# Kernel optimization log

Measured on AMD Instinct MI355X. Metric: run time of the kernel, lower is better.

## Reference

```python
import jax, jax.numpy as jnp
import numpy as np

VOCAB = 50000
EMBED = 256
LABELS = 2
DEPTH = 10          # complete binary tree: 2**DEPTH leaves
B = 256             # batch of trees
L = 2 ** DEPTH      # leaves per tree


def setup_inputs() -> dict:
    key = jax.random.key(0)
    ks = jax.random.split(key, 7)
    token_ids = jax.random.randint(ks[0], (B, L), 0, VOCAB)
    labels = jax.random.randint(ks[1], (B,), 0, LABELS)
    emb = jax.random.normal(ks[2], (VOCAB, EMBED), dtype=jnp.float32)
    W_w = jax.random.normal(ks[3], (EMBED, 2 * EMBED), dtype=jnp.float32) * (1.0 / np.sqrt(2 * EMBED))
    W_b = jax.random.normal(ks[4], (EMBED,), dtype=jnp.float32) * 0.01
    P_w = jax.random.normal(ks[5], (LABELS, EMBED), dtype=jnp.float32) * (1.0 / np.sqrt(EMBED))
    P_b = jax.random.normal(ks[6], (LABELS,), dtype=jnp.float32) * 0.01
    return {"token_ids": token_ids, "labels": labels, "emb": emb,
            "W_w": W_w, "W_b": W_b, "P_w": P_w, "P_b": P_b}


def reference(token_ids, labels, emb, W_w, W_b, P_w, P_b):
    # Leaves: relu(embedding(token))  -> [B, L, E]
    x = jax.nn.relu(emb[token_ids])
    # Level-by-level combine: currentNode = relu(W @ cat(left, right) + b)
    # Leaf order is left-to-right, so adjacent pairs (2k, 2k+1) are siblings;
    # reshape concatenates (left, right) along features, matching torch.cat((l, r), 1).
    while x.shape[1] > 1:
        bsz, n, e = x.shape
        lr = x.reshape(bsz, n // 2, 2 * e)                       # [B, n/2, 2E]
        x = jax.nn.relu(jnp.einsum('bnf,ef->bne', lr, W_w) + W_b)
    root = x[:, 0]                                               # [B, E]
    logits = root @ P_w.T + P_b                                  # [B, label_size]
    prediction = jnp.argmax(logits, axis=1)
    logp = jax.nn.log_softmax(logits, axis=-1)
    loss = -jnp.take_along_axis(logp, labels[:, None], axis=1)[:, 0]  # per-tree CE
    return prediction, loss
```

## Files before the change

kernel.cpp:

```cpp
#include <hip/hip_runtime.h>
#include <hip/hip_bf16.h>
#include <math.h>

#define EMBED   256
#define KDIM    512
#define BATCH   256
#define BM      128
#define VOCAB   50000

typedef float  f32x4   __attribute__((ext_vector_type(4)));
typedef __bf16 bf16x8  __attribute__((ext_vector_type(8)));
typedef unsigned short ushort8 __attribute__((ext_vector_type(8)));

__device__ __forceinline__ unsigned short f2h(float f) {
    unsigned int u = __float_as_uint(f);
    u += 0x7FFFu + ((u >> 16) & 1u);
    return (unsigned short)(u >> 16);
}
__device__ __forceinline__ float h2f(unsigned short h) {
    return __uint_as_float(((unsigned int)h) << 16);
}
__device__ __forceinline__ void gload16(const void* g, void* l) {
    __builtin_amdgcn_global_load_lds(
        (const __attribute__((address_space(1))) unsigned int*)g,
        (__attribute__((address_space(3))) unsigned int*)l, 16, 0, 0);
}

#define MFMA16(a,b,c) __builtin_amdgcn_mfma_f32_16x16x32_bf16((a),(b),(c),0,0,0)

__global__ __launch_bounds__(256) void prep_all(const float* __restrict__ emb,
                                                unsigned short* __restrict__ Eh,
                                                unsigned short* __restrict__ El,
                                                const float* __restrict__ W,
                                                unsigned short* __restrict__ Wh,
                                                unsigned short* __restrict__ Wl,
                                                int wprep)
{
    const int bid = blockIdx.x;
    if (bid < 6250) {
        const size_t base = ((size_t)bid * 256 + threadIdx.x) * 8;
        float v[8];
        *(float4*)&v[0] = *(const float4*)&emb[base];
        *(float4*)&v[4] = *(const float4*)&emb[base + 4];
        ushort8 hs, ls;
        #pragma unroll
        for (int i = 0; i < 8; ++i) {
            const float f = fmaxf(v[i], 0.f);
            const unsigned short h = f2h(f);
            hs[i] = h;
            ls[i] = f2h(f - h2f(h));
        }
        *(ushort8*)&Eh[base] = hs;
        *(ushort8*)&El[base] = ls;
    } else if (wprep) {
        const int i = (bid - 6250) * 256 + threadIdx.x;
        const float w = W[i];
        const unsigned short h = f2h(w);
        Wh[i] = h;
        Wl[i] = f2h(w - h2f(h));
    }
}

template<int LV1, int WPREP>
__global__ __launch_bounds__(512) void gemm_tree(
    const unsigned short* __restrict__ Xh, const unsigned short* __restrict__ Xl,
    const unsigned short* __restrict__ Wh, const unsigned short* __restrict__ Wl,
    const float*  __restrict__ Wf,
    const float*  __restrict__ bias,
    unsigned short* __restrict__ Yh, unsigned short* __restrict__ Yl,
    const int* __restrict__ tok,
    const unsigned short* __restrict__ Eh, const unsigned short* __restrict__ El)
{
    __shared__ __align__(16) unsigned short AhL[4096], AlL[4096];
    __shared__ __align__(16) unsigned short BhL[8192], BlL[8192];

    const int tid = threadIdx.x;
    const int wid = tid >> 6;
    const int l   = tid & 63;
    const int q   = l >> 4;
    const int rr  = l & 15;
    const int m0  = blockIdx.x * BM;

    const int waveM = wid >> 2;
    const int waveN = wid & 3;

    int tk0 = 0, tk1 = 0;
    if constexpr (LV1) {
        const int r = m0 + wid * 16 + rr;
        tk0 = tok[2 * r];
        tk1 = tok[2 * r + 1];
    }

    f32x4 acc[4][4] = {};

    for (int t = 0; t < 16; ++t) {
        const int k0   = t << 5;
        const int joff = k0 >> 8;
        const int c    = (k0 & 255) + q * 8;

        if constexpr (LV1) {
            const size_t off = (size_t)(joff ? tk1 : tk0) * EMBED + c;
            gload16(Eh + off, &AhL[wid * 512]);
            gload16(El + off, &AlL[wid * 512]);
        } else {
            const size_t off = (size_t)(2 * (m0 + wid * 16 + rr) + joff) * EMBED + c;
            gload16(Xh + off, &AhL[wid * 512]);
            gload16(Xl + off, &AlL[wid * 512]);
        }
        #pragma unroll
        for (int g = 0; g < 2; ++g) {
            const int s = wid + g * 8;
            if constexpr (WPREP) {
                const size_t off = (size_t)(s * 16 + rr) * KDIM + k0 + q * 8;
                gload16(Wh + off, &BhL[s * 512]);
                gload16(Wl + off, &BlL[s * 512]);
            } else {
                const float* ws = Wf + (size_t)(s * 16 + rr) * KDIM + k0 + q * 8;
                float v[8];
                *(float4*)&v[0] = *(const float4*)ws;
                *(float4*)&v[4] = *(const float4*)(ws + 4);
                ushort8 hs, ls;
                #pragma unroll
                for (int i = 0; i < 8; ++i) {
                    const unsigned short h = f2h(v[i]);
                    hs[i] = h;
                    ls[i] = f2h(v[i] - h2f(h));
                }
                *(ushort8*)&BhL[s * 512 + l * 8] = hs;
                *(ushort8*)&BlL[s * 512 + l * 8] = ls;
            }
        }

        __syncthreads();

        bf16x8 ah[4], al[4], bh[4], bl[4];
        #pragma unroll
        for (int mi = 0; mi < 4; ++mi) {
            ah[mi] = *(const bf16x8*)&AhL[(waveM * 4 + mi) * 512 + l * 8];
            al[mi] = *(const bf16x8*)&AlL[(waveM * 4 + mi) * 512 + l * 8];
        }
        #pragma unroll
        for (int ni = 0; ni < 4; ++ni) {
            bh[ni] = *(const bf16x8*)&BhL[(waveN * 4 + ni) * 512 + l * 8];
            bl[ni] = *(const bf16x8*)&BlL[(waveN * 4 + ni) * 512 + l * 8];
        }
        #pragma unroll
        for (int mi = 0; mi < 4; ++mi)
            #pragma unroll
            for (int ni = 0; ni < 4; ++ni)
                acc[mi][ni] = MFMA16(ah[mi], bh[ni], acc[mi][ni]);
        #pragma unroll
        for (int mi = 0; mi < 4; ++mi)
            #pragma unroll
            for (int ni = 0; ni < 4; ++ni)
                acc[mi][ni] = MFMA16(al[mi], bh[ni], acc[mi][ni]);
        #pragma unroll
        for (int mi = 0; mi < 4; ++mi)
            #pragma unroll
            for (int ni = 0; ni < 4; ++ni)
                acc[mi][ni] = MFMA16(ah[mi], bl[ni], acc[mi][ni]);

        __syncthreads();
    }

    #pragma unroll
    for (int ni = 0; ni < 4; ++ni) {
        const int col = waveN * 64 + ni * 16 + rr;
        const float bv = bias[col];
        #pragma unroll
        for (int mi = 0; mi < 4; ++mi) {
            const int row0 = m0 + waveM * 64 + mi * 16 + q * 4;
            #pragma unroll
            for (int jj = 0; jj < 4; ++jj) {
                const float y = fmaxf(acc[mi][ni][jj] + bv, 0.f);
                const unsigned short h = f2h(y);
                Yh[(size_t)(row0 + jj) * EMBED + col] = h;
                Yl[(size_t)(row0 + jj) * EMBED + col] = f2h(y - h2f(h));
            }
        }
    }
}

template<int WPREP>
__global__ __launch_bounds__(256) void tail3(
    const unsigned short* __restrict__ A2h, const unsigned short* __restrict__ A2l,
    unsigned short* __restrict__ S3h, unsigned short* __restrict__ S3l,
    const unsigned short* __restrict__ Wh, const unsigned short* __restrict__ Wl,
    const float* __restrict__ Wf, const float* __restrict__ bias,
    const float* __restrict__ Pw, const float* __restrict__ Pb,
    const int* __restrict__ labels, float* __restrict__ out)
{
    __shared__ __align__(16) unsigned short BhT[2][8192], BlT[2][8192];
    __shared__ __align__(16) unsigned short Asth[2][4096], Astl[2][4096];
    __shared__ __align__(16) unsigned short X0h[8192], X0l[8192];
    __shared__ __align__(16) unsigned short X1h[4096], X1l[4096];

    const int tid = threadIdx.x;
    const int w   = tid >> 6;
    const int l   = tid & 63;
    const int q   = l >> 4;
    const int rr  = l & 15;
    const int b   = blockIdx.x;

    unsigned short* L4h = S3h + (size_t)32768 * 256;
    unsigned short* L4l = S3l + (size_t)32768 * 256;

    auto stageB = [&](int buf, int k0) {
        if constexpr (WPREP) {
            #pragma unroll
            for (int j = 0; j < 8; ++j) {
                const int sb = w * 8 + j;
                const int s  = sb & 15;
                const size_t off = (size_t)(s * 16 + rr) * KDIM + k0 + q * 8;
                if (sb < 16) gload16(Wh + off, &BhT[buf][s * 512]);
                else         gload16(Wl + off, &BlT[buf][s * 512]);
            }
        } else {
            #pragma unroll
            for (int j = 0; j < 4; ++j) {
                const int u = w * 4 + j;
                const float* ws = Wf + (size_t)(u * 16 + rr) * KDIM + k0 + q * 8;
                float v[8];
                *(float4*)&v[0] = *(const float4*)ws;
                *(float4*)&v[4] = *(const float4*)(ws + 4);
                ushort8 hs, ls;
                #pragma unroll
                for (int i = 0; i < 8; ++i) {
                    const unsigned short h = f2h(v[i]);
                    hs[i] = h;
                    ls[i] = f2h(v[i] - h2f(h));
                }
                *(ushort8*)&BhT[buf][u * 512 + l * 8] = hs;
                *(ushort8*)&BlT[buf][u * 512 + l * 8] = ls;
            }
        }
    };

    float bv[4];
    #pragma unroll
    for (int ni = 0; ni < 4; ++ni) bv[ni] = bias[w * 64 + ni * 16 + rr];

    int g = 0;

    auto stageA3 = [&](int buf, int t) {
        const int k0 = t * 32, joff = k0 >> 8, c = (k0 & 255) + q * 8;
        #pragma unroll
        for (int j = 0; j < 4; ++j) {
            const int u = w * 4 + j, s = u & 7;
            const size_t off = (size_t)(256 * b + 2 * (s * 16 + rr) + joff) * EMBED + c;
            if (u < 8) gload16(A2h + off, &Asth[buf][s * 512]);
            else       gload16(A2l + off, &Astl[buf][s * 512]);
        }
    };
    stageB(0, 0);
    stageA3(0, 0);
    __syncthreads();
    {
        f32x4 acc[8][4] = {};
        for (int t = 0; t < 16; ++t, ++g) {
            const int cur = g & 1;
            if (g < 127) stageB(cur ^ 1, ((t + 1) & 15) * 32);
            if (t < 15)  stageA3((t + 1) & 1, t + 1);
            bf16x8 bh4[4], bl4[4];
            #pragma unroll
            for (int ni = 0; ni < 4; ++ni) {
                bh4[ni] = *(const bf16x8*)&BhT[cur][(w * 4 + ni) * 512 + l * 8];
                bl4[ni] = *(const bf16x8*)&BlT[cur][(w * 4 + ni) * 512 + l * 8];
            }
            #pragma unroll
            for (int mi = 0; mi < 8; ++mi) {
                const bf16x8 a_h = *(const bf16x8*)&Asth[t & 1][mi * 512 + l * 8];
                const bf16x8 a_l = *(const bf16x8*)&Astl[t & 1][mi * 512 + l * 8];
                #pragma unroll
                for (int ni = 0; ni < 4; ++ni) acc[mi][ni] = MFMA16(a_h, bh4[ni], acc[mi][ni]);
                #pragma unroll
                for (int ni = 0; ni < 4; ++ni) acc[mi][ni] = MFMA16(a_l, bh4[ni], acc[mi][ni]);
                #pragma unroll
                for (int ni = 0; ni < 4; ++ni) acc[mi][ni] = MFMA16(a_h, bl4[ni], acc[mi][ni]);
            }
            __syncthreads();
        }
        #pragma unroll
        for (int ni = 0; ni < 4; ++ni) {
            const int col = w * 64 + ni * 16 + rr;
            #pragma unroll
            for (int mi = 0; mi < 8; ++mi)
                #pragma unroll
                for (int jj = 0; jj < 4; ++jj) {
                    const int row = mi * 16 + q * 4 + jj;
                    const float y = fmaxf(acc[mi][ni][jj] + bv[ni], 0.f);
                    const unsigned short h = f2h(y);
                    S3h[(size_t)(128 * b + row) * EMBED + col] = h;
                    S3l[(size_t)(128 * b + row) * EMBED + col] = f2h(y - h2f(h));
                }
        }
    }
    __syncthreads();

    auto stageA4 = [&](int buf, int t) {
        const int k0 = t * 32, joff = k0 >> 8, c = (k0 & 255) + q * 8;
        #pragma unroll
        for (int j = 0; j < 2; ++j) {
            const int u = w * 2 + j, s = u & 3;
            const size_t off = (size_t)(128 * b + 2 * (s * 16 + rr) + joff) * EMBED + c;
            if (u < 4) gload16(S3h + off, &Asth[buf][s * 512]);
            else       gload16(S3l + off, &Astl[buf][s * 512]);
        }
    };
    stageA4(0, 0);
    {
        f32x4 acc[4][4] = {};
        for (int t = 0; t < 16; ++t, ++g) {
            const int cur = g & 1;
            if (g < 127) stageB(cur ^ 1, ((t + 1) & 15) * 32);
            if (t < 15)  stageA4((t + 1) & 1, t + 1);
            bf16x8 bh4[4], bl4[4];
            #pragma unroll
            for (int ni = 0; ni < 4; ++ni) {
                bh4[ni] = *(const bf16x8*)&BhT[cur][(w * 4 + ni) * 512 + l * 8];
                bl4[ni] = *(const bf16x8*)&BlT[cur][(w * 4 + ni) * 512 + l * 8];
            }
            #pragma unroll
            for (int mi = 0; mi < 4; ++mi) {
                const bf16x8 a_h = *(const bf16x8*)&Asth[t & 1][mi * 512 + l * 8];
                const bf16x8 a_l = *(const bf16x8*)&Astl[t & 1][mi * 512 + l * 8];
                #pragma unroll
                for (int ni = 0; ni < 4; ++ni) acc[mi][ni] = MFMA16(a_h, bh4[ni], acc[mi][ni]);
                #pragma unroll
                for (int ni = 0; ni < 4; ++ni) acc[mi][ni] = MFMA16(a_l, bh4[ni], acc[mi][ni]);
                #pragma unroll
                for (int ni = 0; ni < 4; ++ni) acc[mi][ni] = MFMA16(a_h, bl4[ni], acc[mi][ni]);
            }
            __syncthreads();
        }
        #pragma unroll
        for (int ni = 0; ni < 4; ++ni) {
            const int col = w * 64 + ni * 16 + rr;
            #pragma unroll
            for (int mi = 0; mi < 4; ++mi)
                #pragma unroll
                for (int jj = 0; jj < 4; ++jj) {
                    const int row = mi * 16 + q * 4 + jj;
                    const float y = fmaxf(acc[mi][ni][jj] + bv[ni], 0.f);
                    const unsigned short h = f2h(y);
                    L4h[(size_t)(64 * b + row) * EMBED + col] = h;
                    L4l[(size_t)(64 * b + row) * EMBED + col] = f2h(y - h2f(h));
                }
        }
    }
    __syncthreads();

    auto stageA5 = [&](int buf, int t) {
        const int k0 = t * 32, joff = k0 >> 8, c = (k0 & 255) + q * 8;
        const int u = w, s = u & 1;
        const size_t off = (size_t)(64 * b + 2 * (s * 16 + rr) + joff) * EMBED + c;
        if (u < 2) gload16(L4h + off, &Asth[buf][s * 512]);
        else       gload16(L4l + off, &Astl[buf][s * 512]);
    };
    stageA5(0, 0);
    {
        f32x4 acc[2][4] = {};
        for (int t = 0; t < 16; ++t, ++g) {
            const int cur = g & 1;
            if (g < 127) stageB(cur ^ 1, ((t + 1) & 15) * 32);
            if (t < 15)  stageA5((t + 1) & 1, t + 1);
            bf16x8 bh4[4], bl4[4];
            #pragma unroll
            for (int ni = 0; ni < 4; ++ni) {
                bh4[ni] = *(const bf16x8*)&BhT[cur][(w * 4 + ni) * 512 + l * 8];
                bl4[ni] = *(const bf16x8*)&BlT[cur][(w * 4 + ni) * 512 + l * 8];
            }
            #pragma unroll
            for (int mi = 0; mi < 2; ++mi) {
                const bf16x8 a_h = *(const bf16x8*)&Asth[t & 1][mi * 512 + l * 8];
                const bf16x8 a_l = *(const bf16x8*)&Astl[t & 1][mi * 512 + l * 8];
                #pragma unroll
                for (int ni = 0; ni < 4; ++ni) acc[mi][ni] = MFMA16(a_h, bh4[ni], acc[mi][ni]);
                #pragma unroll
                for (int ni = 0; ni < 4; ++ni) acc[mi][ni] = MFMA16(a_l, bh4[ni], acc[mi][ni]);
                #pragma unroll
                for (int ni = 0; ni < 4; ++ni) acc[mi][ni] = MFMA16(a_h, bl4[ni], acc[mi][ni]);
            }
            __syncthreads();
        }
        #pragma unroll
        for (int ni = 0; ni < 4; ++ni) {
            const int col = w * 64 + ni * 16 + rr;
            #pragma unroll
            for (int mi = 0; mi < 2; ++mi)
                #pragma unroll
                for (int jj = 0; jj < 4; ++jj) {
                    const int row = mi * 16 + q * 4 + jj;
                    const float y = fmaxf(acc[mi][ni][jj] + bv[ni], 0.f);
                    const unsigned short h = f2h(y);
                    const int idx = (row * 256 + col) ^ ((row & 7) << 3);
                    X0h[idx] = h;
                    X0l[idx] = f2h(y - h2f(h));
                }
        }
    }
    __syncthreads();

    for (int s = 1; s < 6; ++s) {
        unsigned short* srch = (s & 1) ? X0h : X1h;
        unsigned short* srcl = (s & 1) ? X0l : X1l;
        unsigned short* dsth = (s & 1) ? X1h : X0h;
        unsigned short* dstl = (s & 1) ? X1l : X0l;
        const int Mout = 32 >> s;

        f32x4 acc[4] = {};
        for (int t = 0; t < 16; ++t, ++g) {
            const int cur = g & 1;
            if (g < 127) stageB(cur ^ 1, ((t + 1) & 15) * 32);

            const int k0   = t * 32;
            const int joff = k0 >> 8;
            const int c    = (k0 & 255) + q * 8;
            const int row  = 2 * rr + joff;
            const int idx  = (row * 256 + c) ^ ((row & 7) << 3);
            const bf16x8 a_h = *(const bf16x8*)&srch[idx];
            const bf16x8 a_l = *(const bf16x8*)&srcl[idx];

            bf16x8 bh4[4], bl4[4];
            #pragma unroll
            for (int ni = 0; ni < 4; ++ni) {
                bh4[ni] = *(const bf16x8*)&BhT[cur][(w * 4 + ni) * 512 + l * 8];
                bl4[ni] = *(const bf16x8*)&BlT[cur][(w * 4 + ni) * 512 + l * 8];
            }
            #pragma unroll
            for (int ni = 0; ni < 4; ++ni) acc[ni] = MFMA16(a_h, bh4[ni], acc[ni]);
            #pragma unroll
            for (int ni = 0; ni < 4; ++ni) acc[ni] = MFMA16(a_l, bh4[ni], acc[ni]);
            #pragma unroll
            for (int ni = 0; ni < 4; ++ni) acc[ni] = MFMA16(a_h, bl4[ni], acc[ni]);

            __syncthreads();
        }

        #pragma unroll
        for (int ni = 0; ni < 4; ++ni) {
            const int col = w * 64 + ni * 16 + rr;
            #pragma unroll
            for (int jj = 0; jj < 4; ++jj) {
                const int row = q * 4 + jj;
                if (row < Mout) {
                    const float y = fmaxf(acc[ni][jj] + bv[ni], 0.f);
                    const unsigned short h = f2h(y);
                    const int idx = (row * 256 + col) ^ ((row & 7) << 3);
                    dsth[idx] = h;
                    dstl[idx] = f2h(y - h2f(h));
                }
            }
        }
        __syncthreads();
    }

    if (w == 0) {
        float s0 = 0.f, s1 = 0.f;
        #pragma unroll
        for (int i = 0; i < 4; ++i) {
            const int col = l + i * 64;
            const float x = h2f(X1h[col]) + h2f(X1l[col]);
            s0 = fmaf(x, Pw[col], s0);
            s1 = fmaf(x, Pw[EMBED + col], s1);
        }
        #pragma unroll
        for (int off = 32; off > 0; off >>= 1) {
            s0 += __shfl_down(s0, off);
            s1 += __shfl_down(s1, off);
        }
        if (l == 0) {
            const float l0 = s0 + Pb[0];
            const float l1 = s1 + Pb[1];
            const int pred = (l1 > l0) ? 1 : 0;
            const float m  = fmaxf(l0, l1);
            const float lse = m + logf(expf(l0 - m) + expf(l1 - m));
            const int lab = labels[b];
            out[b]         = (float)pred;
            out[BATCH + b] = lse - (lab ? l1 : l0);
        }
    }
}

extern "C" void kernel_launch(void* const* d_in, const int* in_sizes, int n_in,
                              void* d_out, int out_size, void* d_ws, size_t ws_size,
                              hipStream_t stream)
{
    const int*   token_ids = (const int*)d_in[0];
    const int*   labels    = (const int*)d_in[1];
    const float* emb       = (const float*)d_in[2];
    const float* W_w       = (const float*)d_in[3];
    const float* W_b       = (const float*)d_in[4];
    const float* P_w       = (const float*)d_in[5];
    const float* P_b       = (const float*)d_in[6];
    float*       out       = (float*)d_out;

    unsigned short* Ah_buf = (unsigned short*)d_ws;
    unsigned short* Al_buf = Ah_buf + (size_t)131072 * 256;
    unsigned short* Bh_buf = Al_buf + (size_t)131072 * 256;
    unsigned short* Bl_buf = Bh_buf + (size_t)65536 * 256;
    unsigned short* Wh     = Bl_buf + (size_t)65536 * 256;
    unsigned short* Wl     = Wh + 131072;
    unsigned short* Eh     = Bh_buf;
    unsigned short* El     = Bl_buf;

    const size_t need_wprep = ((size_t)131072 * 256 * 2 + (size_t)65536 * 256 * 2 + 2 * 131072) * 2;
    const bool wprep = ws_size >= need_wprep;

    prep_all<<<6762, 256, 0, stream>>>(emb, Eh, El, W_w, Wh, Wl, wprep ? 1 : 0);

    if (wprep) {
        gemm_tree<1,1><<<1024, 512, 0, stream>>>(nullptr, nullptr, Wh, Wl, W_w, W_b, Ah_buf, Al_buf, token_ids, Eh, El);
        gemm_tree<0,1><<< 512, 512, 0, stream>>>(Ah_buf, Al_buf, Wh, Wl, W_w, W_b, Bh_buf, Bl_buf, nullptr, nullptr, nullptr);
        tail3<1><<<BATCH, 256, 0, stream>>>(Bh_buf, Bl_buf, Ah_buf, Al_buf, Wh, Wl, W_w, W_b, P_w, P_b, labels, out);
    } else {
        gemm_tree<1,0><<<1024, 512, 0, stream>>>(nullptr, nullptr, Wh, Wl, W_w, W_b, Ah_buf, Al_buf, token_ids, Eh, El);
        gemm_tree<0,0><<< 512, 512, 0, stream>>>(Ah_buf, Al_buf, Wh, Wl, W_w, W_b, Bh_buf, Bl_buf, nullptr, nullptr, nullptr);
        tail3<0><<<BATCH, 256, 0, stream>>>(Bh_buf, Bl_buf, Ah_buf, Al_buf, Wh, Wl, W_w, W_b, P_w, P_b, labels, out);
    }
}
```

Baseline: 409.6 us.

## Widen tail kernel to 8 waves and load operands directly into registers

The per-tree tail kernel now launches 512 threads (8 waves) instead of 256 and splits each level's GEMM across a 2x4 wave grid in M and N. The LDS double-buffered staging of weights and activations is removed, and each wave now reads W and A fragments straight from global memory into registers, which also drops the per-step __syncthreads. The aim is more parallelism per tree and less barrier overhead. In exchange, every wave re-reads the weights from global or cache with no LDS reuse, and the small tree levels split the N dimension across all 8 waves.

```diff
diff --git a/kernel.cpp b/kernel.cpp
--- a/kernel.cpp
+++ b/kernel.cpp
@@ -182,7 +182,7 @@
 }
 
 template<int WPREP>
-__global__ __launch_bounds__(256) void tail3(
+__global__ __launch_bounds__(512) void tail3(
     const unsigned short* __restrict__ A2h, const unsigned short* __restrict__ A2l,
     unsigned short* __restrict__ S3h, unsigned short* __restrict__ S3l,
     const unsigned short* __restrict__ Wh, const unsigned short* __restrict__ Wl,
@@ -190,8 +190,6 @@
     const float* __restrict__ Pw, const float* __restrict__ Pb,
     const int* __restrict__ labels, float* __restrict__ out)
 {
-    __shared__ __align__(16) unsigned short BhT[2][8192], BlT[2][8192];
-    __shared__ __align__(16) unsigned short Asth[2][4096], Astl[2][4096];
     __shared__ __align__(16) unsigned short X0h[8192], X0l[8192];
     __shared__ __align__(16) unsigned short X1h[4096], X1l[4096];
 
@@ -205,21 +203,18 @@
     unsigned short* L4h = S3h + (size_t)32768 * 256;
     unsigned short* L4l = S3l + (size_t)32768 * 256;
 
-    auto stageB = [&](int buf, int k0) {
-        if constexpr (WPREP) {
-            #pragma unroll
-            for (int j = 0; j < 8; ++j) {
-                const int sb = w * 8 + j;
-                const int s  = sb & 15;
-                const size_t off = (size_t)(s * 16 + rr) * KDIM + k0 + q * 8;
-                if (sb < 16) gload16(Wh + off, &BhT[buf][s * 512]);
-                else         gload16(Wl + off, &BlT[buf][s * 512]);
-            }
-        } else {
-            #pragma unroll
-            for (int j = 0; j < 4; ++j) {
-                const int u = w * 4 + j;
-                const float* ws = Wf + (size_t)(u * 16 + rr) * KDIM + k0 + q * 8;
+    const int waveM = w >> 2;
+    const int waveN = w & 3;
+
+    auto loadB4 = [&](int colb, int k0, bf16x8* bh, bf16x8* bl) {
+        #pragma unroll
+        for (int ni = 0; ni < 4; ++ni) {
+            const size_t off = (size_t)(colb + ni * 16 + rr) * KDIM + k0 + q * 8;
+            if constexpr (WPREP) {
+                bh[ni] = *(const bf16x8*)&Wh[off];
+                bl[ni] = *(const bf16x8*)&Wl[off];
+            } else {
+                const float* ws = Wf + off;
                 float v[8];
                 *(float4*)&v[0] = *(const float4*)ws;
                 *(float4*)&v[4] = *(const float4*)(ws + 4);
@@ -230,65 +225,45 @@
                     hs[i] = h;
                     ls[i] = f2h(v[i] - h2f(h));
                 }
-                *(ushort8*)&BhT[buf][u * 512 + l * 8] = hs;
-                *(ushort8*)&BlT[buf][u * 512 + l * 8] = ls;
+                bh[ni] = __builtin_bit_cast(bf16x8, hs);
+                bl[ni] = __builtin_bit_cast(bf16x8, ls);
             }
         }
     };
 
-    float bv[4];
+    float bv4[4];
     #pragma unroll
-    for (int ni = 0; ni < 4; ++ni) bv[ni] = bias[w * 64 + ni * 16 + rr];
-
-    int g = 0;
-
-    auto stageA3 = [&](int buf, int t) {
-        const int k0 = t * 32, joff = k0 >> 8, c = (k0 & 255) + q * 8;
-        #pragma unroll
-        for (int j = 0; j < 4; ++j) {
-            const int u = w * 4 + j, s = u & 7;
-            const size_t off = (size_t)(256 * b + 2 * (s * 16 + rr) + joff) * EMBED + c;
-            if (u < 8) gload16(A2h + off, &Asth[buf][s * 512]);
-            else       gload16(A2l + off, &Astl[buf][s * 512]);
-        }
-    };
-    stageB(0, 0);
-    stageA3(0, 0);
-    __syncthreads();
+    for (int ni = 0; ni < 4; ++ni) bv4[ni] = bias[waveN * 64 + ni * 16 + rr];
+
     {
-        f32x4 acc[8][4] = {};
-        for (int t = 0; t < 16; ++t, ++g) {
-            const int cur = g & 1;
-            if (g < 127) stageB(cur ^ 1, ((t + 1) & 15) * 32);
-            if (t < 15)  stageA3((t + 1) & 1, t + 1);
-            bf16x8 bh4[4], bl4[4];
-            #pragma unroll
-            for (int ni = 0; ni < 4; ++ni) {
-                bh4[ni] = *(const bf16x8*)&BhT[cur][(w * 4 + ni) * 512 + l * 8];
-                bl4[ni] = *(const bf16x8*)&BlT[cur][(w * 4 + ni) * 512 + l * 8];
-            }
-            #pragma unroll
-            for (int mi = 0; mi < 8; ++mi) {
-                const bf16x8 a_h = *(const bf16x8*)&Asth[t & 1][mi * 512 + l * 8];
-                const bf16x8 a_l = *(const bf16x8*)&Astl[t & 1][mi * 512 + l * 8];
-                #pragma unroll
-                for (int ni = 0; ni < 4; ++ni) acc[mi][ni] = MFMA16(a_h, bh4[ni], acc[mi][ni]);
-                #pragma unroll
-                for (int ni = 0; ni < 4; ++ni) acc[mi][ni] = MFMA16(a_l, bh4[ni], acc[mi][ni]);
-                #pragma unroll
-                for (int ni = 0; ni < 4; ++ni) acc[mi][ni] = MFMA16(a_h, bl4[ni], acc[mi][ni]);
-            }
-            __syncthreads();
+        f32x4 acc[4][4] = {};
+        #pragma unroll 2
+        for (int t = 0; t < 16; ++t) {
+            const int k0 = t * 32, joff = t >> 3, c = (k0 & 255) + q * 8;
+            bf16x8 bh[4], bl[4];
+            loadB4(waveN * 64, k0, bh, bl);
+            #pragma unroll
+            for (int mi = 0; mi < 4; ++mi) {
+                const size_t ar = (size_t)(256 * b + 2 * (waveM * 64 + mi * 16 + rr) + joff) * EMBED + c;
+                const bf16x8 a_h = *(const bf16x8*)&A2h[ar];
+                const bf16x8 a_l = *(const bf16x8*)&A2l[ar];
+                #pragma unroll
+                for (int ni = 0; ni < 4; ++ni) acc[mi][ni] = MFMA16(a_h, bh[ni], acc[mi][ni]);
+                #pragma unroll
+                for (int ni = 0; ni < 4; ++ni) acc[mi][ni] = MFMA16(a_l, bh[ni], acc[mi][ni]);
+                #pragma unroll
+                for (int ni = 0; ni < 4; ++ni) acc[mi][ni] = MFMA16(a_h, bl[ni], acc[mi][ni]);
+            }
         }
         #pragma unroll
         for (int ni = 0; ni < 4; ++ni) {
-            const int col = w * 64 + ni * 16 + rr;
-            #pragma unroll
-            for (int mi = 0; mi < 8; ++mi)
+            const int col = waveN * 64 + ni * 16 + rr;
+            #pragma unroll
+            for (int mi = 0; mi < 4; ++mi)
                 #pragma unroll
                 for (int jj = 0; jj < 4; ++jj) {
-                    const int row = mi * 16 + q * 4 + jj;
-                    const float y = fmaxf(acc[mi][ni][jj] + bv[ni], 0.f);
+                    const int row = waveM * 64 + mi * 16 + q * 4 + jj;
+                    const float y = fmaxf(acc[mi][ni][jj] + bv4[ni], 0.f);
                     const unsigned short h = f2h(y);
                     S3h[(size_t)(128 * b + row) * EMBED + col] = h;
                     S3l[(size_t)(128 * b + row) * EMBED + col] = f2h(y - h2f(h));
@@ -297,51 +272,35 @@
     }
     __syncthreads();
 
-    auto stageA4 = [&](int buf, int t) {
-        const int k0 = t * 32, joff = k0 >> 8, c = (k0 & 255) + q * 8;
-        #pragma unroll
-        for (int j = 0; j < 2; ++j) {
-            const int u = w * 2 + j, s = u & 3;
-            const size_t off = (size_t)(128 * b + 2 * (s * 16 + rr) + joff) * EMBED + c;
-            if (u < 4) gload16(S3h + off, &Asth[buf][s * 512]);
-            else       gload16(S3l + off, &Astl[buf][s * 512]);
-        }
-    };
-    stageA4(0, 0);
     {
-        f32x4 acc[4][4] = {};
-        for (int t = 0; t < 16; ++t, ++g) {
-            const int cur = g & 1;
-            if (g < 127) stageB(cur ^ 1, ((t + 1) & 15) * 32);
-            if (t < 15)  stageA4((t + 1) & 1, t + 1);
-            bf16x8 bh4[4], bl4[4];
-            #pragma unroll
-            for (int ni = 0; ni < 4; ++ni) {
-                bh4[ni] = *(const bf16x8*)&BhT[cur][(w * 4 + ni) * 512 + l * 8];
-                bl4[ni] = *(const bf16x8*)&BlT[cur][(w * 4 + ni) * 512 + l * 8];
-            }
-            #pragma unroll
-            for (int mi = 0; mi < 4; ++mi) {
-                const bf16x8 a_h = *(const bf16x8*)&Asth[t & 1][mi * 512 + l * 8];
-                const bf16x8 a_l = *(const bf16x8*)&Astl[t & 1][mi * 512 + l * 8];
-                #pragma unroll
-                for (int ni = 0; ni < 4; ++ni) acc[mi][ni] = MFMA16(a_h, bh4[ni], acc[mi][ni]);
-                #pragma unroll
-                for (int ni = 0; ni < 4; ++ni) acc[mi][ni] = MFMA16(a_l, bh4[ni], acc[mi][ni]);
-                #pragma unroll
-                for (int ni = 0; ni < 4; ++ni) acc[mi][ni] = MFMA16(a_h, bl4[ni], acc[mi][ni]);
-            }
-            __syncthreads();
+        f32x4 acc[2][4] = {};
+        #pragma unroll 2
+        for (int t = 0; t < 16; ++t) {
+            const int k0 = t * 32, joff = t >> 3, c = (k0 & 255) + q * 8;
+            bf16x8 bh[4], bl[4];
+            loadB4(waveN * 64, k0, bh, bl);
+            #pragma unroll
+            for (int mi = 0; mi < 2; ++mi) {
+                const size_t ar = (size_t)(128 * b + 2 * (waveM * 32 + mi * 16 + rr) + joff) * EMBED + c;
+                const bf16x8 a_h = *(const bf16x8*)&S3h[ar];
+                const bf16x8 a_l = *(const bf16x8*)&S3l[ar];
+                #pragma unroll
+                for (int ni = 0; ni < 4; ++ni) acc[mi][ni] = MFMA16(a_h, bh[ni], acc[mi][ni]);
+                #pragma unroll
+                for (int ni = 0; ni < 4; ++ni) acc[mi][ni] = MFMA16(a_l, bh[ni], acc[mi][ni]);
+                #pragma unroll
+                for (int ni = 0; ni < 4; ++ni) acc[mi][ni] = MFMA16(a_h, bl[ni], acc[mi][ni]);
+            }
         }
         #pragma unroll
         for (int ni = 0; ni < 4; ++ni) {
-            const int col = w * 64 + ni * 16 + rr;
-            #pragma unroll
-            for (int mi = 0; mi < 4; ++mi)
+            const int col = waveN * 64 + ni * 16 + rr;
+            #pragma unroll
+            for (int mi = 0; mi < 2; ++mi)
                 #pragma unroll
                 for (int jj = 0; jj < 4; ++jj) {
-                    const int row = mi * 16 + q * 4 + jj;
-                    const float y = fmaxf(acc[mi][ni][jj] + bv[ni], 0.f);
+                    const int row = waveM * 32 + mi * 16 + q * 4 + jj;
+                    const float y = fmaxf(acc[mi][ni][jj] + bv4[ni], 0.f);
                     const unsigned short h = f2h(y);
                     L4h[(size_t)(64 * b + row) * EMBED + col] = h;
                     L4l[(size_t)(64 * b + row) * EMBED + col] = f2h(y - h2f(h));
@@ -350,101 +309,98 @@
     }
     __syncthreads();
 
-    auto stageA5 = [&](int buf, int t) {
-        const int k0 = t * 32, joff = k0 >> 8, c = (k0 & 255) + q * 8;
-        const int u = w, s = u & 1;
-        const size_t off = (size_t)(64 * b + 2 * (s * 16 + rr) + joff) * EMBED + c;
-        if (u < 2) gload16(L4h + off, &Asth[buf][s * 512]);
-        else       gload16(L4l + off, &Astl[buf][s * 512]);
-    };
-    stageA5(0, 0);
     {
-        f32x4 acc[2][4] = {};
-        for (int t = 0; t < 16; ++t, ++g) {
-            const int cur = g & 1;
-            if (g < 127) stageB(cur ^ 1, ((t + 1) & 15) * 32);
-            if (t < 15)  stageA5((t + 1) & 1, t + 1);
-            bf16x8 bh4[4], bl4[4];
-            #pragma unroll
-            for (int ni = 0; ni < 4; ++ni) {
-                bh4[ni] = *(const bf16x8*)&BhT[cur][(w * 4 + ni) * 512 + l * 8];
-                bl4[ni] = *(const bf16x8*)&BlT[cur][(w * 4 + ni) * 512 + l * 8];
-            }
-            #pragma unroll
-            for (int mi = 0; mi < 2; ++mi) {
-                const bf16x8 a_h = *(const bf16x8*)&Asth[t & 1][mi * 512 + l * 8];
-                const bf16x8 a_l = *(const bf16x8*)&Astl[t & 1][mi * 512 + l * 8];
-                #pragma unroll
-                for (int ni = 0; ni < 4; ++ni) acc[mi][ni] = MFMA16(a_h, bh4[ni], acc[mi][ni]);
-                #pragma unroll
-                for (int ni = 0; ni < 4; ++ni) acc[mi][ni] = MFMA16(a_l, bh4[ni], acc[mi][ni]);
-                #pragma unroll
-                for (int ni = 0; ni < 4; ++ni) acc[mi][ni] = MFMA16(a_h, bl4[ni], acc[mi][ni]);
-            }
-            __syncthreads();
+        f32x4 acc[4] = {};
+        #pragma unroll 4
+        for (int t = 0; t < 16; ++t) {
+            const int k0 = t * 32, joff = t >> 3, c = (k0 & 255) + q * 8;
+            bf16x8 bh[4], bl[4];
+            loadB4(waveN * 64, k0, bh, bl);
+            const size_t ar = (size_t)(64 * b + 2 * (waveM * 16 + rr) + joff) * EMBED + c;
+            const bf16x8 a_h = *(const bf16x8*)&L4h[ar];
+            const bf16x8 a_l = *(const bf16x8*)&L4l[ar];
+            #pragma unroll
+            for (int ni = 0; ni < 4; ++ni) acc[ni] = MFMA16(a_h, bh[ni], acc[ni]);
+            #pragma unroll
+            for (int ni = 0; ni < 4; ++ni) acc[ni] = MFMA16(a_l, bh[ni], acc[ni]);
+            #pragma unroll
+            for (int ni = 0; ni < 4; ++ni) acc[ni] = MFMA16(a_h, bl[ni], acc[ni]);
         }
         #pragma unroll
         for (int ni = 0; ni < 4; ++ni) {
-            const int col = w * 64 + ni * 16 + rr;
-            #pragma unroll
-            for (int mi = 0; mi < 2; ++mi)
-                #pragma unroll
-                for (int jj = 0; jj < 4; ++jj) {
-                    const int row = mi * 16 + q * 4 + jj;
-                    const float y = fmaxf(acc[mi][ni][jj] + bv[ni], 0.f);
-                    const unsigned short h = f2h(y);
-                    const int idx = (row * 256 + col) ^ ((row & 7) << 3);
-                    X0h[idx] = h;
-                    X0l[idx] = f2h(y - h2f(h));
-                }
+            const int col = waveN * 64 + ni * 16 + rr;
+            #pragma unroll
+            for (int jj = 0; jj < 4; ++jj) {
+                const int row = waveM * 16 + q * 4 + jj;
+                const float y = fmaxf(acc[ni][jj] + bv4[ni], 0.f);
+                const unsigned short h = f2h(y);
+                const int idx = (row * 256 + col) ^ ((row & 7) << 3);
+                X0h[idx] = h;
+                X0l[idx] = f2h(y - h2f(h));
+            }
         }
     }
     __syncthreads();
 
-    for (int s = 1; s < 6; ++s) {
-        unsigned short* srch = (s & 1) ? X0h : X1h;
-        unsigned short* srcl = (s & 1) ? X0l : X1l;
-        unsigned short* dsth = (s & 1) ? X1h : X0h;
-        unsigned short* dstl = (s & 1) ? X1l : X0l;
-        const int Mout = 32 >> s;
-
-        f32x4 acc[4] = {};
-        for (int t = 0; t < 16; ++t, ++g) {
-            const int cur = g & 1;
-            if (g < 127) stageB(cur ^ 1, ((t + 1) & 15) * 32);
-
-            const int k0   = t * 32;
-            const int joff = k0 >> 8;
-            const int c    = (k0 & 255) + q * 8;
-            const int row  = 2 * rr + joff;
-            const int idx  = (row * 256 + c) ^ ((row & 7) << 3);
+    float bv2[2];
+    #pragma unroll
+    for (int ni = 0; ni < 2; ++ni) bv2[ni] = bias[w * 32 + ni * 16 + rr];
+
+    for (int s = 0; s < 5; ++s) {
+        const unsigned short* srch = (s & 1) ? X1h : X0h;
+        const unsigned short* srcl = (s & 1) ? X1l : X0l;
+        unsigned short* dsth = (s & 1) ? X0h : X1h;
+        unsigned short* dstl = (s & 1) ? X0l : X1l;
+        const int mask = (s & 1) ? 15 : 31;
+        const int Mout = 16 >> s;
+
+        f32x4 acc[2] = {};
+        #pragma unroll 4
+        for (int t = 0; t < 16; ++t) {
+            const int k0 = t * 32, joff = t >> 3, c = (k0 & 255) + q * 8;
+            const int row = (2 * rr + joff) & mask;
+            const int idx = (row * 256 + c) ^ ((row & 7) << 3);
             const bf16x8 a_h = *(const bf16x8*)&srch[idx];
             const bf16x8 a_l = *(const bf16x8*)&srcl[idx];
-
-            bf16x8 bh4[4], bl4[4];
-            #pragma unroll
-            for (int ni = 0; ni < 4; ++ni) {
-                bh4[ni] = *(const bf16x8*)&BhT[cur][(w * 4 + ni) * 512 + l * 8];
-                bl4[ni] = *(const bf16x8*)&BlT[cur][(w * 4 + ni) * 512 + l * 8];
-            }
-            #pragma unroll
-            for (int ni = 0; ni < 4; ++ni) acc[ni] = MFMA16(a_h, bh4[ni], acc[ni]);
-            #pragma unroll
-            for (int ni = 0; ni < 4; ++ni) acc[ni] = MFMA16(a_l, bh4[ni], acc[ni]);
-            #pragma unroll
-            for (int ni = 0; ni < 4; ++ni) acc[ni] = MFMA16(a_h, bl4[ni], acc[ni]);
-
-            __syncthreads();
-        }
-
-        #pragma unroll
-        for (int ni = 0; ni < 4; ++ni) {
-            const int col = w * 64 + ni * 16 + rr;
+            bf16x8 bh[2], bl[2];
+            #pragma unroll
+            for (int ni = 0; ni < 2; ++ni) {
+                const size_t off = (size_t)(w * 32 + ni * 16 + rr) * KDIM + k0 + q * 8;
+                if constexpr (WPREP) {
+                    bh[ni] = *(const bf16x8*)&Wh[off];
+                    bl[ni] = *(const bf16x8*)&Wl[off];
+                } else {
+                    const float* ws = Wf + off;
+                    float v[8];
+                    *(float4*)&v[0] = *(const float4*)ws;
+                    *(float4*)&v[4] = *(const float4*)(ws + 4);
+                    ushort8 hs, ls;
+                    #pragma unroll
+                    for (int i = 0; i < 8; ++i) {
+                        const unsigned short h = f2h(v[i]);
+                        hs[i] = h;
+                        ls[i] = f2h(v[i] - h2f(h));
+                    }
+                    bh[ni] = __builtin_bit_cast(bf16x8, hs);
+                    bl[ni] = __builtin_bit_cast(bf16x8, ls);
+                }
+            }
+            #pragma unroll
+            for (int ni = 0; ni < 2; ++ni) acc[ni] = MFMA16(a_h, bh[ni], acc[ni]);
+            #pragma unroll
+            for (int ni = 0; ni < 2; ++ni) acc[ni] = MFMA16(a_l, bh[ni], acc[ni]);
+            #pragma unroll
+            for (int ni = 0; ni < 2; ++ni) acc[ni] = MFMA16(a_h, bl[ni], acc[ni]);
+        }
+
+        #pragma unroll
+        for (int ni = 0; ni < 2; ++ni) {
+            const int col = w * 32 + ni * 16 + rr;
             #pragma unroll
             for (int jj = 0; jj < 4; ++jj) {
                 const int row = q * 4 + jj;
                 if (row < Mout) {
-                    const float y = fmaxf(acc[ni][jj] + bv[ni], 0.f);
+                    const float y = fmaxf(acc[ni][jj] + bv2[ni], 0.f);
                     const unsigned short h = f2h(y);
                     const int idx = (row * 256 + col) ^ ((row & 7) << 3);
                     dsth[idx] = h;
@@ -512,10 +468,10 @@
     if (wprep) {
         gemm_tree<1,1><<<1024, 512, 0, stream>>>(nullptr, nullptr, Wh, Wl, W_w, W_b, Ah_buf, Al_buf, token_ids, Eh, El);
         gemm_tree<0,1><<< 512, 512, 0, stream>>>(Ah_buf, Al_buf, Wh, Wl, W_w, W_b, Bh_buf, Bl_buf, nullptr, nullptr, nullptr);
-        tail3<1><<<BATCH, 256, 0, stream>>>(Bh_buf, Bl_buf, Ah_buf, Al_buf, Wh, Wl, W_w, W_b, P_w, P_b, labels, out);
+        tail3<1><<<BATCH, 512, 0, stream>>>(Bh_buf, Bl_buf, Ah_buf, Al_buf, Wh, Wl, W_w, W_b, P_w, P_b, labels, out);
     } else {
         gemm_tree<1,0><<<1024, 512, 0, stream>>>(nullptr, nullptr, Wh, Wl, W_w, W_b, Ah_buf, Al_buf, token_ids, Eh, El);
         gemm_tree<0,0><<< 512, 512, 0, stream>>>(Ah_buf, Al_buf, Wh, Wl, W_w, W_b, Bh_buf, Bl_buf, nullptr, nullptr, nullptr);
-        tail3<0><<<BATCH, 256, 0, stream>>>(Bh_buf, Bl_buf, Ah_buf, Al_buf, Wh, Wl, W_w, W_b, P_w, P_b, labels, out);
-    }
-}
+        tail3<0><<<BATCH, 512, 0, stream>>>(Bh_buf, Bl_buf, Ah_buf, Al_buf, Wh, Wl, W_w, W_b, P_w, P_b, labels, out);
+    }
+}
```

Result: slower. 455.8 us (+11.3%).
